# Performance work log

Measured on AMD Instinct MI355X. Metric: run time of the kernel, lower is better.

Reference implementation:

```python
import jax, jax.numpy as jnp
import numpy as np

B, L, D, H = 2, 2048, 1024, 16
DH = D // H
SCALE = DH ** -0.5


def setup_inputs() -> dict:
    key = jax.random.key(0)
    k1, k2, k3 = jax.random.split(key, 3)
    x = jax.random.normal(k1, (B, L, D), dtype=jnp.float32)
    W_qkv = jax.random.normal(k2, (D, 3 * D), dtype=jnp.float32) * 0.02
    b_qkv = jnp.zeros((3 * D,), dtype=jnp.float32)
    W_proj = jax.random.normal(k3, (D, D), dtype=jnp.float32) * 0.02
    b_proj = jnp.zeros((D,), dtype=jnp.float32)
    return {"x": x, "W_qkv": W_qkv, "b_qkv": b_qkv, "W_proj": W_proj, "b_proj": b_proj}


def reference(x, W_qkv, b_qkv, W_proj, b_proj):
    b, l, d = x.shape
    # QKV projection: [B,L,3D] -> [3,B,H,L,DH] matching 'b n (three h d) -> three b h n d'
    qkv = (x @ W_qkv + b_qkv).reshape(b, l, 3, H, DH).transpose(2, 0, 3, 1, 4)
    q, k, v = qkv[0], qkv[1], qkv[2]
    # Causal scores. Chunking in the original is purely a scheduling detail;
    # masks are indexed by absolute row positions, so full attention is identical.
    scores = jnp.einsum('bhqd,bhkd->bhqk', q, k) * SCALE
    mask = jnp.triu(jnp.ones((l, l), dtype=bool), 1)  # True above diagonal
    neg_inf = jnp.finfo(scores.dtype).min
    scores = jnp.where(mask, neg_inf, scores)
    m = jnp.max(scores, axis=-1, keepdims=True)
    e = jnp.where(mask, 0.0, jnp.exp(scores - m))
    attn = e / (jnp.sum(e, axis=-1, keepdims=True) + 1e-6)
    out = jnp.einsum('bhqk,bhkd->bhqd', attn, v)  # [B,H,L,DH]
    out = out.transpose(0, 2, 1, 3).reshape(b, l, d)  # 'b h n d -> b n (h d)'
    return out @ W_proj + b_proj
```

## Files before the change

### kernel.cpp

```cpp
#include <hip/hip_runtime.h>


typedef __bf16 bf16x8 __attribute__((ext_vector_type(8)));
typedef float  f32x4  __attribute__((ext_vector_type(4)));
typedef unsigned short bhalf;
typedef unsigned int   uint32;

#define B_  2
#define L_  2048
#define D_  1024
#define H_  16
#define DH_ 64

#define GPTR(p) ((const __attribute__((address_space(1))) void*)(p))
#define SPTR(p) ((__attribute__((address_space(3))) void*)(p))

static __device__ __forceinline__ float bf2f(bhalf u) {
    union { uint32 u; float f; } x; x.u = ((uint32)u) << 16; return x.f;
}
static __device__ __forceinline__ bhalf f2bf(float f) {
    union { float f; uint32 u; } x; x.f = f;
    uint32 r = x.u + 0x7FFFu + ((x.u >> 16) & 1u);
    return (bhalf)(r >> 16);
}

__global__ void detect_dtype(const uint32* __restrict__ xw, int* __restrict__ flag) {
    int t = threadIdx.x;
    uint32 w = xw[t];
    uint32 e = (w >> 7) & 0xFFu;
    int g = (e < 0x6Fu || e > 0x84u) ? 1 : 0;
#pragma unroll
    for (int off = 32; off; off >>= 1) g += __shfl_xor(g, off);
    if (t == 0) *flag = (g > 16) ? 0 : 1;
}

__global__ void conv_bf16(const void* __restrict__ in, bhalf* __restrict__ out,
                          int n4, const int* __restrict__ flag) {
    const bool isb = (*flag != 0);
    for (int i = blockIdx.x * blockDim.x + threadIdx.x; i < n4;
         i += gridDim.x * blockDim.x) {
        if (isb) {
            ((uint2*)out)[i] = ((const uint2*)in)[i];
        } else {
            float4 v = ((const float4*)in)[i];
            uint2 o;
            o.x = (uint32)f2bf(v.x) | ((uint32)f2bf(v.y) << 16);
            o.y = (uint32)f2bf(v.z) | ((uint32)f2bf(v.w) << 16);
            ((uint2*)out)[i] = o;
        }
    }
}

__global__ void tr_conv(const void* __restrict__ in, bhalf* __restrict__ out,
                        int R, int C, const int* __restrict__ flag) {
    __shared__ bhalf t[32][33];
    const bool isb = (*flag != 0);
    int bx = blockIdx.x, by = blockIdx.y;
    int tx = threadIdx.x, ty = threadIdx.y;
#pragma unroll
    for (int i = 0; i < 32; i += 8) {
        size_t idx = (size_t)(by * 32 + ty + i) * C + bx * 32 + tx;
        t[ty + i][tx] = isb ? ((const bhalf*)in)[idx]
                            : f2bf(((const float*)in)[idx]);
    }
    __syncthreads();
#pragma unroll
    for (int i = 0; i < 32; i += 8)
        out[(size_t)(bx * 32 + ty + i) * R + by * 32 + tx] = t[tx][ty + i];
}


#define GSTAGE(BUF, KK) do {                                                  \
    int kko = (KK);                                                           \
    int bufv = (BUF);                                                         \
    _Pragma("unroll")                                                         \
    for (int r = 0; r < 2; r++) {                                             \
        int c = r * 256 + tid;                                                \
        int row = c >> 2, p = c & 3;                                          \
        int gch = (p - row - (row >> 2)) & 3;                                 \
        __builtin_amdgcn_global_load_lds(                                     \
            GPTR(a0 + (size_t)row * K + kko + gch * 8),                       \
            SPTR(As + bufv * 4096 + (r * 256 + w * 64) * 8), 16, 0, 0);       \
        __builtin_amdgcn_global_load_lds(                                     \
            GPTR(b0 + (size_t)row * K + kko + gch * 8),                       \
            SPTR(Bs + bufv * 4096 + (r * 256 + w * 64) * 8), 16, 0, 0);       \
    }                                                                         \
} while (0)

template <int MODE>
__global__ __launch_bounds__(256) void gemm_bt(
        const bhalf* __restrict__ A, const bhalf* __restrict__ Bt,
        const void* __restrict__ bias,
        void* __restrict__ C0, bhalf* __restrict__ Qb,
        bhalf* __restrict__ Kb, bhalf* __restrict__ Vtb,
        int M, int N, int K, const int* __restrict__ flag) {
    __shared__ bhalf As[3 * 128 * 32];
    __shared__ bhalf Bs[3 * 128 * 32];
    const bool isb = (*flag != 0);
    const int tid  = threadIdx.x;
    const int w    = tid >> 6, lane = tid & 63;
    const int g    = lane >> 4, cl = lane & 15;
    const int m0   = blockIdx.y * 128, n0 = blockIdx.x * 128;
    const int wr   = (w >> 1) * 64, wc = (w & 1) * 64;

    f32x4 acc[4][4] = {};

    const bhalf* a0 = A  + (size_t)m0 * K;
    const bhalf* b0 = Bt + (size_t)n0 * K;

    const int nk = K >> 5;
    GSTAGE(0, 0);
    GSTAGE(1, 32);

    for (int t = 0; t < nk; ++t) {
        asm volatile("s_waitcnt vmcnt(4)" ::: "memory");
        __builtin_amdgcn_sched_barrier(0);
        __builtin_amdgcn_s_barrier();
        __builtin_amdgcn_sched_barrier(0);

        int tp = t + 2 < nk ? t + 2 : nk - 1;
        GSTAGE((t + 2) % 3, tp << 5);

        int cur = t % 3;
        bf16x8 af[4], bf4[4];
#pragma unroll
        for (int i = 0; i < 4; i++) {
            int ra = wr + i * 16 + cl;
            af[i]  = *(const bf16x8*)(As + cur * 4096 + ra * 32 +
                                      (((g + ra + (ra >> 2)) & 3) * 8));
            int rb = wc + i * 16 + cl;
            bf4[i] = *(const bf16x8*)(Bs + cur * 4096 + rb * 32 +
                                      (((g + rb + (rb >> 2)) & 3) * 8));
        }
        __builtin_amdgcn_s_setprio(1);
#pragma unroll
        for (int i = 0; i < 4; i++)
#pragma unroll
            for (int j = 0; j < 4; j++)
                acc[i][j] = __builtin_amdgcn_mfma_f32_16x16x32_bf16(
                    af[i], bf4[j], acc[i][j], 0, 0, 0);
        __builtin_amdgcn_s_setprio(0);
    }

#pragma unroll
    for (int i = 0; i < 4; i++) {
#pragma unroll
        for (int j = 0; j < 4; j++) {
            int nn = n0 + wc + j * 16 + cl;
            float bv = isb ? bf2f(((const bhalf*)bias)[nn])
                           : ((const float*)bias)[nn];
#pragma unroll
            for (int r = 0; r < 4; r++) {
                int mm = m0 + wr + i * 16 + g * 4 + r;
                float v = acc[i][j][r] + bv;
                if (MODE == 0) {
                    if (isb) ((bhalf*)C0)[(size_t)mm * N + nn] = f2bf(v);
                    else     ((float*)C0)[(size_t)mm * N + nn] = v;
                } else {
                    int b = mm >> 11, l = mm & 2047;
                    int three = nn >> 10, rem = nn & 1023;
                    int h = rem >> 6, dh = rem & 63;
                    size_t bh = (size_t)(b * 16 + h);
                    if (three == 0) {
                        Qb[(bh * 2048 + l) * 64 + dh] = f2bf(v * 0.18033688f);
                    } else if (three == 1) {
                        Kb [(bh * 2048 + l) * 64 + dh] = f2bf(v);
                    } else {
                        Vtb[(bh * 64 + dh) * 2048 + l] = f2bf(v);
                    }
                }
            }
        }
    }
}


#define STAGE(BUF, KT) do {                                                   \
    int ktv = (KT);                                                           \
    _Pragma("unroll")                                                         \
    for (int r = 0; r < 4; r++) {                                             \
        int c = r * 256 + tid;                                                \
        int row = c >> 3, p = c & 7;                                          \
        int fsw = (row & 3) | (((row >> 3) & 1) << 2);                        \
        __builtin_amdgcn_global_load_lds(                                     \
            GPTR(Kp + (size_t)(ktv * 128 + row) * 64 + (p ^ fsw) * 8),        \
            SPTR(Ks[BUF] + (r * 256 + w * 64) * 8), 16, 0, 0);                \
    }                                                                         \
    _Pragma("unroll")                                                         \
    for (int r = 0; r < 4; r++) {                                             \
        int c = r * 256 + tid;                                                \
        int row = c >> 4, p = c & 15;                                         \
        __builtin_amdgcn_global_load_lds(                                     \
            GPTR(Vt + (size_t)row * L_ + ktv * 128 + (p ^ (row & 15)) * 8),   \
            SPTR(Vs[BUF] + (r * 256 + w * 64) * 8), 16, 0, 0);                \
    }                                                                         \
} while (0)

#define ATTN_TILE(BUF, KT, QF, QLANE, MVAR, LVAR, OACC, MASK) do {            \
    f32x4 p8[8] = {};                                                         \
    _Pragma("unroll")                                                         \
    for (int s = 0; s < 2; s++) {                                             \
        bf16x8 kf[8];                                                         \
        _Pragma("unroll")                                                     \
        for (int j = 0; j < 8; j++) {                                         \
            int row = (j >> 1) * 32 + (cl >> 2) * 8 + (j & 1) * 4 + (cl & 3); \
            int fsw = (row & 3) | (((row >> 3) & 1) << 2);                    \
            int ch = s * 4 + g;                                               \
            kf[j] = *(const bf16x8*)(Ks[BUF] + row * 64 + ((ch ^ fsw) * 8));  \
        }                                                                     \
        __builtin_amdgcn_s_setprio(1);                                        \
        _Pragma("unroll")                                                     \
        for (int j = 0; j < 8; j++)                                           \
            p8[j] = __builtin_amdgcn_mfma_f32_16x16x32_bf16(                  \
                kf[j], QF[s], p8[j], 0, 0, 0);                                \
        __builtin_amdgcn_s_setprio(0);                                        \
    }                                                                         \
    float mx0 = -__builtin_inff(), mx1 = -__builtin_inff();                   \
    float mx2 = -__builtin_inff(), mx3 = -__builtin_inff();                   \
    _Pragma("unroll")                                                         \
    for (int j = 0; j < 8; j++) {                                             \
        float v0 = p8[j][0], v1 = p8[j][1], v2 = p8[j][2], v3 = p8[j][3];     \
        if (MASK) {                                                           \
            int ka = (KT) * 128 + (j >> 1) * 32 + g * 8 + ((j & 1) << 2);     \
            v0 = (ka + 0 > (QLANE)) ? -__builtin_inff() : v0;                 \
            v1 = (ka + 1 > (QLANE)) ? -__builtin_inff() : v1;                 \
            v2 = (ka + 2 > (QLANE)) ? -__builtin_inff() : v2;                 \
            v3 = (ka + 3 > (QLANE)) ? -__builtin_inff() : v3;                 \
            p8[j][0] = v0; p8[j][1] = v1; p8[j][2] = v2; p8[j][3] = v3;       \
        }                                                                     \
        mx0 = fmaxf(mx0, v0); mx1 = fmaxf(mx1, v1);                           \
        mx2 = fmaxf(mx2, v2); mx3 = fmaxf(mx3, v3);                           \
    }                                                                         \
    float mx = fmaxf(fmaxf(mx0, mx1), fmaxf(mx2, mx3));                       \
    mx = fmaxf(mx, __shfl_xor(mx, 16));                                       \
    mx = fmaxf(mx, __shfl_xor(mx, 32));                                       \
    if (!__all(mx - MVAR <= 8.f)) {       \
        float mnew = fmaxf(MVAR, mx);                                         \
        float alpha = __builtin_amdgcn_exp2f(MVAR - mnew);                    \
        MVAR = mnew;                                                          \
        LVAR *= alpha;                                                        \
        _Pragma("unroll")                                                     \
        for (int r = 0; r < 4; r++) {                                         \
            float ar = __shfl(alpha, g * 4 + r);                              \
            _Pragma("unroll")                                                 \
            for (int dj = 0; dj < 4; dj++) OACC[dj][r] *= ar;                 \
        }                                                                     \
    }                                                                         \
    float s0 = 0.f, s1 = 0.f, s2 = 0.f, s3 = 0.f;                             \
    _Pragma("unroll")                                                         \
    for (int j = 0; j < 8; j++) {                                             \
        float e0 = __builtin_amdgcn_exp2f(p8[j][0] - MVAR);                   \
        float e1 = __builtin_amdgcn_exp2f(p8[j][1] - MVAR);                   \
        float e2 = __builtin_amdgcn_exp2f(p8[j][2] - MVAR);                   \
        float e3 = __builtin_amdgcn_exp2f(p8[j][3] - MVAR);                   \
        p8[j][0] = e0; p8[j][1] = e1; p8[j][2] = e2; p8[j][3] = e3;           \
        s0 += e0; s1 += e1; s2 += e2; s3 += e3;                               \
    }                                                                         \
    float ls = (s0 + s1) + (s2 + s3);                                         \
    ls += __shfl_xor(ls, 16);                                                 \
    ls += __shfl_xor(ls, 32);                                                 \
    LVAR += ls;                                                               \
    _Pragma("unroll")                                                         \
    for (int ks = 0; ks < 4; ks++) {                                          \
        bf16x8 pf;                                                            \
        _Pragma("unroll")                                                     \
        for (int e = 0; e < 8; e++)                                           \
            pf[e] = (__bf16)p8[2 * ks + (e >> 2)][e & 3];                     \
        bf16x8 vf[4];                                                         \
        _Pragma("unroll")                                                     \
        for (int dj = 0; dj < 4; dj++) {                                      \
            int vrow = dj * 16 + cl;                                          \
            int ch = ks * 4 + g;                                              \
            vf[dj] = *(const bf16x8*)(Vs[BUF] + vrow * 128 + ((ch ^ (vrow & 15)) * 8)); \
        }                                                                     \
        __builtin_amdgcn_s_setprio(1);                                        \
        _Pragma("unroll")                                                     \
        for (int dj = 0; dj < 4; dj++)                                        \
            OACC[dj] = __builtin_amdgcn_mfma_f32_16x16x32_bf16(               \
                pf, vf[dj], OACC[dj], 0, 0, 0);                               \
        __builtin_amdgcn_s_setprio(0);                                        \
    }                                                                         \
} while (0)

__global__ __launch_bounds__(256, 2) void attn_fwd(
        const bhalf* __restrict__ Qb, const bhalf* __restrict__ Kb,
        const bhalf* __restrict__ Vtb, bhalf* __restrict__ Ob) {
    __shared__ bhalf Ks[2][128 * 64];
    __shared__ bhalf Vs[2][64 * 128];

    const int bid  = blockIdx.x;
    const int xcd  = bid & 7, slot = bid >> 3;
    const int bx   = slot & 15;
    const int bh   = xcd + 8 * (slot >> 4);
    const int qbA  = 31 - bx;
    const int qbB  = bx;

    const int tid = threadIdx.x;
    const int w = tid >> 6, lane = tid & 63;
    const int g = lane >> 4, cl = lane & 15;

    const bhalf* Q  = Qb  + (size_t)bh * L_ * DH_;
    const bhalf* Kp = Kb  + (size_t)bh * L_ * DH_;
    const bhalf* Vt = Vtb + (size_t)bh * DH_ * L_;

    const int q0A = qbA * 64 + w * 16, qlA = q0A + cl;
    const int q0B = qbB * 64 + w * 16, qlB = q0B + cl;

    bf16x8 qfA[2], qfB[2];
#pragma unroll
    for (int s = 0; s < 2; s++) {
        qfA[s] = *(const bf16x8*)(Q + (size_t)(q0A + cl) * 64 + s * 32 + g * 8);
        qfB[s] = *(const bf16x8*)(Q + (size_t)(q0B + cl) * 64 + s * 32 + g * 8);
    }

    f32x4 oA[4] = {}, oB[4] = {};
    float mA = -__builtin_inff(), lA = 0.f;
    float mB = -__builtin_inff(), lB = 0.f;

    const int nktA = (qbA >> 1) + 1;
    const int nktB = (qbB >> 1) + 1;

    STAGE(0, 0);
    __syncthreads();

    for (int kt = 0; kt < nktA; ++kt) {
        int cur = kt & 1;
        if (kt + 1 < nktA) STAGE(cur ^ 1, kt + 1);
        if (kt < nktB) {
            ATTN_TILE(cur, kt, qfB, qlB, mB, lB, oB, (kt == nktB - 1));
        }
        ATTN_TILE(cur, kt, qfA, qlA, mA, lA, oA, (kt == nktA - 1));
        __syncthreads();
    }

    const int b = bh >> 4, h = bh & 15;
#pragma unroll
    for (int r = 0; r < 4; r++) {
        float lrA = __shfl(lA, g * 4 + r);
        float lrB = __shfl(lB, g * 4 + r);
        float invA = 1.f / (lrA + 1e-6f);
        float invB = 1.f / (lrB + 1e-6f);
        int qrA = q0A + g * 4 + r, qrB = q0B + g * 4 + r;
#pragma unroll
        for (int dj = 0; dj < 4; dj++) {
            Ob[((size_t)b * L_ + qrA) * D_ + h * 64 + dj * 16 + cl] =
                f2bf(oA[dj][r] * invA);
            Ob[((size_t)b * L_ + qrB) * D_ + h * 64 + dj * 16 + cl] =
                f2bf(oB[dj][r] * invB);
        }
    }
}

extern "C" void kernel_launch(void* const* d_in, const int* in_sizes, int n_in,
                              void* d_out, int out_size, void* d_ws, size_t ws_size,
                              hipStream_t stream) {
    const void* x     = d_in[0];
    const void* Wqkv  = d_in[1];
    const void* bqkv  = d_in[2];
    const void* Wproj = d_in[3];
    const void* bproj = d_in[4];

    char* ws = (char*)d_ws;
    const size_t SZ_FLG = 256;
    const size_t SZ_WQT = (size_t)3 * D_ * D_ * 2;
    const size_t SZ_WPT = (size_t)D_ * D_ * 2;
    const size_t SZ_X   = (size_t)B_ * L_ * D_ * 2;
    const size_t SZ_BUF = (size_t)B_ * H_ * L_ * DH_ * 2;

    int*   flag = (int*)ws;
    bhalf* Wq_t = (bhalf*)(ws + SZ_FLG);
    bhalf* Wp_t = (bhalf*)(ws + SZ_FLG + SZ_WQT);
    bhalf* Xb   = (bhalf*)(ws + SZ_FLG + SZ_WQT + SZ_WPT);
    bhalf* Qbuf = (bhalf*)(ws + SZ_FLG + SZ_WQT + SZ_WPT + SZ_X);
    bhalf* Kbuf = (bhalf*)(ws + SZ_FLG + SZ_WQT + SZ_WPT + SZ_X + SZ_BUF);
    bhalf* Vtbf = (bhalf*)(ws + SZ_FLG + SZ_WQT + SZ_WPT + SZ_X + 2 * SZ_BUF);
    bhalf* Obuf = (bhalf*)(ws + SZ_FLG + SZ_WQT + SZ_WPT + SZ_X + 3 * SZ_BUF);

    const int M = B_ * L_;

    detect_dtype<<<1, 64, 0, stream>>>((const uint32*)x, flag);

    conv_bf16<<<2048, 256, 0, stream>>>(x, Xb, (B_ * L_ * D_) / 4, flag);
    tr_conv<<<dim3(3 * D_ / 32, D_ / 32), dim3(32, 8), 0, stream>>>(
        Wqkv, Wq_t, D_, 3 * D_, flag);
    tr_conv<<<dim3(D_ / 32, D_ / 32), dim3(32, 8), 0, stream>>>(
        Wproj, Wp_t, D_, D_, flag);

    gemm_bt<1><<<dim3(3 * D_ / 128, M / 128), 256, 0, stream>>>(
        Xb, Wq_t, bqkv, nullptr, Qbuf, Kbuf, Vtbf, M, 3 * D_, D_, flag);

    attn_fwd<<<dim3(512), 256, 0, stream>>>(Qbuf, Kbuf, Vtbf, Obuf);

    gemm_bt<0><<<dim3(D_ / 128, M / 128), 256, 0, stream>>>(
        Obuf, Wp_t, bproj, d_out, nullptr, nullptr, nullptr, M, D_, D_, flag);
}
```

Before: 127.8 us.

## Add 256x192-tile 512-thread QKV GEMM kernel with split-phase double buffering

Replaces the templated 128x128 QKV projection GEMM with a dedicated kernel that uses 256x192 tiles, 512 threads (8 waves), double-buffered LDS, and loads split into two halves so each half overlaps a batch of MFMAs. The grid shrinks from 24x32 to 16x16 blocks, which raises operand reuse per block and cuts global traffic. The cost is fewer blocks (256) for the device's CUs and more register pressure from 24 accumulators per wave. The output projection stays on the old kernel, now renamed and stripped of the QKV scatter path.

```diff
diff --git a/kernel.cpp b/kernel.cpp
--- a/kernel.cpp
+++ b/kernel.cpp
@@ -69,6 +69,142 @@
         out[(size_t)(bx * 32 + ty + i) * R + by * 32 + tx] = t[tx][ty + i];
 }
 
+__global__ __launch_bounds__(512, 2) void gemm_qkv256(
+        const bhalf* __restrict__ A, const bhalf* __restrict__ Bt,
+        const void* __restrict__ bias,
+        bhalf* __restrict__ Qb, bhalf* __restrict__ Kb, bhalf* __restrict__ Vtb,
+        int K, const int* __restrict__ flag) {
+    __shared__ bhalf As[2][256 * 32];
+    __shared__ bhalf Bs[2][192 * 32];
+    const bool isb = (*flag != 0);
+    const int tid = threadIdx.x;
+    const int w = tid >> 6, lane = tid & 63;
+    const int g = lane >> 4, cl = lane & 15;
+    const int wr = w >> 2, wc = w & 3;
+    const int m0 = blockIdx.y * 256, n0 = blockIdx.x * 192;
+
+    const bhalf* a0 = A  + (size_t)m0 * K;
+    const bhalf* b0 = Bt + (size_t)n0 * K;
+
+    f32x4 acc[8][3] = {};
+
+#define ST_A(BUF, KK, R) do {                                                 \
+    int c = (R) * 512 + tid;                                                  \
+    int row = c >> 2, p = c & 3;                                              \
+    int gch = (p - row - (row >> 2)) & 3;                                     \
+    __builtin_amdgcn_global_load_lds(                                         \
+        GPTR(a0 + (size_t)row * K + (KK) + gch * 8),                          \
+        SPTR(&As[BUF][((R) * 512 + (w << 6)) * 8]), 16, 0, 0);                \
+} while (0)
+#define ST_B0(BUF, KK) do {                                                   \
+    int c = tid;                                                              \
+    int row = c >> 2, p = c & 3;                                              \
+    int gch = (p - row - (row >> 2)) & 3;                                     \
+    __builtin_amdgcn_global_load_lds(                                         \
+        GPTR(b0 + (size_t)row * K + (KK) + gch * 8),                          \
+        SPTR(&Bs[BUF][(w << 6) * 8]), 16, 0, 0);                              \
+} while (0)
+#define ST_B1(BUF, KK) do {                                                   \
+    if (tid < 256) {                        \
+        int c = 512 + tid;                                                    \
+        int row = c >> 2, p = c & 3;                                          \
+        int gch = (p - row - (row >> 2)) & 3;                                 \
+        __builtin_amdgcn_global_load_lds(                                     \
+            GPTR(b0 + (size_t)row * K + (KK) + gch * 8),                      \
+            SPTR(&Bs[BUF][(512 + (w << 6)) * 8]), 16, 0, 0);                  \
+    }                                                                         \
+} while (0)
+
+    const int NT = K >> 5;
+    ST_A(0, 0, 0); ST_A(0, 0, 1); ST_B0(0, 0); ST_B1(0, 0);
+    asm volatile("s_waitcnt vmcnt(0)" ::: "memory");
+    __builtin_amdgcn_s_barrier();
+
+    for (int t = 0; t < NT; ++t) {
+        const int cur = t & 1;
+        const int kn = ((t + 1 < NT) ? t + 1 : NT - 1) << 5;
+        bf16x8 af[4], bf[3];
+
+        ST_A(cur ^ 1, kn, 0);
+        ST_B0(cur ^ 1, kn);
+        asm volatile("s_waitcnt vmcnt(2)" ::: "memory");
+        __builtin_amdgcn_sched_barrier(0);
+        __builtin_amdgcn_s_barrier();
+        __builtin_amdgcn_sched_barrier(0);
+#pragma unroll
+        for (int n = 0; n < 3; n++) {
+            int rb = wc * 48 + n * 16 + cl;
+            bf[n] = *(const bf16x8*)(&Bs[cur][rb * 32 +
+                                     (((g + rb + (rb >> 2)) & 3) * 8)]);
+        }
+#pragma unroll
+        for (int m = 0; m < 4; m++) {
+            int ra = wr * 128 + m * 16 + cl;
+            af[m] = *(const bf16x8*)(&As[cur][ra * 32 +
+                                     (((g + ra + (ra >> 2)) & 3) * 8)]);
+        }
+        asm volatile("s_waitcnt lgkmcnt(0)" ::: "memory");
+        __builtin_amdgcn_sched_barrier(0);
+        __builtin_amdgcn_s_setprio(1);
+#pragma unroll
+        for (int m = 0; m < 4; m++)
+#pragma unroll
+            for (int n = 0; n < 3; n++)
+                acc[m][n] = __builtin_amdgcn_mfma_f32_16x16x32_bf16(
+                    af[m], bf[n], acc[m][n], 0, 0, 0);
+        __builtin_amdgcn_s_setprio(0);
+        __builtin_amdgcn_s_barrier();
+
+        ST_A(cur ^ 1, kn, 1);
+        ST_B1(cur ^ 1, kn);
+#pragma unroll
+        for (int m = 0; m < 4; m++) {
+            int ra = wr * 128 + 64 + m * 16 + cl;
+            af[m] = *(const bf16x8*)(&As[cur][ra * 32 +
+                                     (((g + ra + (ra >> 2)) & 3) * 8)]);
+        }
+        asm volatile("s_waitcnt lgkmcnt(0)" ::: "memory");
+        __builtin_amdgcn_sched_barrier(0);
+        __builtin_amdgcn_s_setprio(1);
+#pragma unroll
+        for (int m = 0; m < 4; m++)
+#pragma unroll
+            for (int n = 0; n < 3; n++)
+                acc[4 + m][n] = __builtin_amdgcn_mfma_f32_16x16x32_bf16(
+                    af[m], bf[n], acc[4 + m][n], 0, 0, 0);
+        __builtin_amdgcn_s_setprio(0);
+        __builtin_amdgcn_s_barrier();
+    }
+#undef ST_A
+#undef ST_B0
+#undef ST_B1
+
+#pragma unroll
+    for (int mi = 0; mi < 8; mi++) {
+#pragma unroll
+        for (int n = 0; n < 3; n++) {
+            int nn = n0 + wc * 48 + n * 16 + cl;
+            float bv = isb ? bf2f(((const bhalf*)bias)[nn])
+                           : ((const float*)bias)[nn];
+#pragma unroll
+            for (int r = 0; r < 4; r++) {
+                int mm = m0 + wr * 128 + (mi >> 2) * 64 + (mi & 3) * 16 + g * 4 + r;
+                float v = acc[mi][n][r] + bv;
+                int b = mm >> 11, l = mm & 2047;
+                int three = nn >> 10, rem = nn & 1023;
+                int h = rem >> 6, dh = rem & 63;
+                size_t bh = (size_t)(b * 16 + h);
+                if (three == 0) {
+                    Qb[(bh * 2048 + l) * 64 + dh] = f2bf(v * 0.18033688f);
+                } else if (three == 1) {
+                    Kb [(bh * 2048 + l) * 64 + dh] = f2bf(v);
+                } else {
+                    Vtb[(bh * 64 + dh) * 2048 + l] = f2bf(v);
+                }
+            }
+        }
+    }
+}
 
 #define GSTAGE(BUF, KK) do {                                                  \
     int kko = (KK);                                                           \
@@ -87,12 +223,9 @@
     }                                                                         \
 } while (0)
 
-template <int MODE>
-__global__ __launch_bounds__(256) void gemm_bt(
+__global__ __launch_bounds__(256) void gemm_proj(
         const bhalf* __restrict__ A, const bhalf* __restrict__ Bt,
-        const void* __restrict__ bias,
-        void* __restrict__ C0, bhalf* __restrict__ Qb,
-        bhalf* __restrict__ Kb, bhalf* __restrict__ Vtb,
+        const void* __restrict__ bias, void* __restrict__ C0,
         int M, int N, int K, const int* __restrict__ flag) {
     __shared__ bhalf As[3 * 128 * 32];
     __shared__ bhalf Bs[3 * 128 * 32];
@@ -153,27 +286,12 @@
             for (int r = 0; r < 4; r++) {
                 int mm = m0 + wr + i * 16 + g * 4 + r;
                 float v = acc[i][j][r] + bv;
-                if (MODE == 0) {
-                    if (isb) ((bhalf*)C0)[(size_t)mm * N + nn] = f2bf(v);
-                    else     ((float*)C0)[(size_t)mm * N + nn] = v;
-                } else {
-                    int b = mm >> 11, l = mm & 2047;
-                    int three = nn >> 10, rem = nn & 1023;
-                    int h = rem >> 6, dh = rem & 63;
-                    size_t bh = (size_t)(b * 16 + h);
-                    if (three == 0) {
-                        Qb[(bh * 2048 + l) * 64 + dh] = f2bf(v * 0.18033688f);
-                    } else if (three == 1) {
-                        Kb [(bh * 2048 + l) * 64 + dh] = f2bf(v);
-                    } else {
-                        Vtb[(bh * 64 + dh) * 2048 + l] = f2bf(v);
-                    }
-                }
+                if (isb) ((bhalf*)C0)[(size_t)mm * N + nn] = f2bf(v);
+                else     ((float*)C0)[(size_t)mm * N + nn] = v;
             }
         }
     }
 }
-
 
 #define STAGE(BUF, KT) do {                                                   \
     int ktv = (KT);                                                           \
@@ -234,7 +352,7 @@
     float mx = fmaxf(fmaxf(mx0, mx1), fmaxf(mx2, mx3));                       \
     mx = fmaxf(mx, __shfl_xor(mx, 16));                                       \
     mx = fmaxf(mx, __shfl_xor(mx, 32));                                       \
-    if (!__all(mx - MVAR <= 8.f)) {       \
+    if (!__all(mx - MVAR <= 8.f)) {                                           \
         float mnew = fmaxf(MVAR, mx);                                         \
         float alpha = __builtin_amdgcn_exp2f(MVAR - mnew);                    \
         MVAR = mnew;                                                          \
@@ -386,11 +504,11 @@
     tr_conv<<<dim3(D_ / 32, D_ / 32), dim3(32, 8), 0, stream>>>(
         Wproj, Wp_t, D_, D_, flag);
 
-    gemm_bt<1><<<dim3(3 * D_ / 128, M / 128), 256, 0, stream>>>(
-        Xb, Wq_t, bqkv, nullptr, Qbuf, Kbuf, Vtbf, M, 3 * D_, D_, flag);
+    gemm_qkv256<<<dim3(3 * D_ / 192, M / 256), 512, 0, stream>>>(
+        Xb, Wq_t, bqkv, Qbuf, Kbuf, Vtbf, D_, flag);
 
     attn_fwd<<<dim3(512), 256, 0, stream>>>(Qbuf, Kbuf, Vtbf, Obuf);
 
-    gemm_bt<0><<<dim3(D_ / 128, M / 128), 256, 0, stream>>>(
-        Obuf, Wp_t, bproj, d_out, nullptr, nullptr, nullptr, M, D_, D_, flag);
-}
+    gemm_proj<<<dim3(D_ / 128, M / 128), 256, 0, stream>>>(
+        Obuf, Wp_t, bproj, d_out, M, D_, D_, flag);
+}
```

Measured after the change: 146.3 us, median of 3. 1.14x slower.
